# Performance work log

Measured on AMD Instinct MI355X. Metric: run time of the kernel, lower is better.

Reference implementation:

```python
import jax, jax.numpy as jnp
import numpy as np

B, T, C, HS, E, NR, P = 2, 2048, 1024, 64, 8, 6, 4
H = C // HS
FF = 4 * C
NT = E - NR


def _ln(x, w, b):
    m = x.mean(-1, keepdims=True)
    v = x.var(-1, keepdims=True)
    return (x - m) * jax.lax.rsqrt(v + 1e-5) * w + b


def _rwkv_scan(r, k, v, w):
    # r,k,v,w: (B,T,H,D); per-head linear-attention recurrence with channel decay
    def step(S, inp):
        r_t, k_t, v_t, w_t = inp  # (B,H,D)
        S = S * w_t[..., :, None] + k_t[..., :, None] * v_t[..., None, :]
        y = jnp.einsum('bhk,bhkv->bhv', r_t, S)
        return S, y
    Bb, Tt, Hh, Dd = r.shape
    S0 = jnp.zeros((Bb, Hh, Dd, Dd), r.dtype)
    xs = tuple(jnp.moveaxis(a, 1, 0) for a in (r, k, v, w))
    _, ys = jax.lax.scan(step, S0, xs)
    return jnp.moveaxis(ys, 0, 1)


def setup_inputs() -> dict:
    key = jax.random.key(0)
    ks = jax.random.split(key, 24)
    s = 1.0 / np.sqrt(C)
    n = lambda k, sh, sc: jax.random.normal(k, sh, jnp.float32) * sc
    return {
        'x': n(ks[0], (B, T, C), 1.0),
        'v_first': jnp.zeros((B, T, C), jnp.float32),
        'capital_shares': jax.random.uniform(ks[1], (E,), dtype=jnp.float32),
        'ln1_w': jnp.ones((C,), jnp.float32), 'ln1_b': jnp.zeros((C,), jnp.float32),
        'ln2_w': jnp.ones((C,), jnp.float32), 'ln2_b': jnp.zeros((C,), jnp.float32),
        'Wr': n(ks[2], (C, C), s), 'Wk': n(ks[3], (C, C), s),
        'Wv': n(ks[4], (C, C), s), 'Ww': n(ks[5], (C, C), s),
        'w_bias': 2.0 * jnp.ones((C,), jnp.float32),
        'Wo': n(ks[6], (C, C), s),
        'conf_w': n(ks[7], (E, C), s), 'conf_b': jnp.zeros((E,), jnp.float32),
        'Wd': n(ks[8], (C, 1), s), 'bd': jnp.zeros((1,), jnp.float32),
        'Wa': n(ks[9], (C, E), s), 'ba': jnp.zeros((E,), jnp.float32),
        'Wb': n(ks[10], (2 * C, P * C), 1.0 / np.sqrt(2 * C)),
        'ffn_Wr': n(ks[11], (NR, C, C), s),
        'ffn_Wk': n(ks[12], (NR, C, FF), s),
        'ffn_Wv': n(ks[13], (NR, FF, C), 1.0 / np.sqrt(FF)),
        'tr_Wq': n(ks[14], (NT, C, C), s), 'tr_Wk': n(ks[15], (NT, C, C), s),
        'tr_Wv': n(ks[16], (NT, C, C), s), 'tr_Wo': n(ks[17], (NT, C, C), s),
    }


def _forward(x, v_first, capital_shares, ln1_w, ln1_b, ln2_w, ln2_b,
             Wr, Wk, Wv, Ww, w_bias, Wo, conf_w, conf_b, Wd, bd, Wa, ba, Wb,
             ffn_Wr, ffn_Wk, ffn_Wv, tr_Wq, tr_Wk, tr_Wv, tr_Wo):
    # --- attention stage: ln1 -> RWKV7 TimeMix -> residual -> ln2 ---
    x_ln = _ln(x, ln1_w, ln1_b)
    r = (x_ln @ Wr).reshape(B, T, H, HS)
    k = (x_ln @ Wk).reshape(B, T, H, HS)
    v_flat = x_ln @ Wv
    v = v_flat.reshape(B, T, H, HS)
    w = jax.nn.sigmoid(x_ln @ Ww + w_bias).reshape(B, T, H, HS)  # decay in (0,1)
    rwkv_state = _rwkv_scan(r, k, v, w).reshape(B, T, C)
    att_out = rwkv_state @ Wo
    x_after_att = x + att_out
    h = _ln(x_after_att, ln2_w, ln2_b)
    # --- no-grad market routing: confidences + critic + top-2 auction ---
    rh = jax.lax.stop_gradient(h)
    conf = jax.nn.sigmoid(jnp.einsum('btc,ec->bte', rh, conf_w) + conf_b)  # (B,T,E)
    difficulty = jax.nn.softplus(rh @ Wd + bd)          # (B,T,1)
    affinity = rh @ Wa + ba                             # (B,T,E)
    subsidy = jax.nn.softmax(affinity, axis=-1)         # critic subsidy
    bids = conf * capital_shares + subsidy
    top_vals, winners = jax.lax.top_k(bids, 2)          # (B,T,2)
    weights = jax.lax.stop_gradient(jax.nn.softmax(top_vals, axis=-1))
    # --- bridge prefix for transformer experts ---
    BT = B * T
    flat_h = h.reshape(BT, C)
    flat_state = rwkv_state.reshape(BT, C)
    prefix = jnp.tanh(jnp.concatenate([flat_h, flat_state], -1) @ Wb).reshape(BT, P, C)
    # --- top-2 expert mixing: gate==0 for unselected tokens (same math as masked dispatch) ---
    final_out = jnp.zeros_like(h)
    scale = 1.0 / np.sqrt(HS)
    for e in range(E):
        gate = (weights * (winners == e)).sum(-1)  # (B,T)
        if e < NR:  # sparse RWKV FFN expert: relu^2 channel-mix with receptance gate
            kk = jax.nn.relu(h @ ffn_Wk[e]) ** 2
            out_e = jax.nn.sigmoid(h @ ffn_Wr[e]) * (kk @ ffn_Wv[e])
        else:       # linear transformer expert: cross-attend token over its bridge prefix
            t = e - NR
            q = (flat_h @ tr_Wq[t]).reshape(BT, H, HS)
            kp = (prefix @ tr_Wk[t]).reshape(BT, P, H, HS)
            vp = (prefix @ tr_Wv[t]).reshape(BT, P, H, HS)
            a = jax.nn.softmax(jnp.einsum('nhd,nphd->nhp', q, kp) * scale, -1)
            out_e = (jnp.einsum('nhp,nphd->nhd', a, vp).reshape(BT, C) @ tr_Wo[t]).reshape(B, T, C)
        final_out = final_out + gate[..., None] * out_e
    x_out = x_after_att + final_out
    return x_out, v_flat  # layer 0: v_first is set to the value projection


def reference(x, v_first, capital_shares, ln1_w, ln1_b, ln2_w, ln2_b,
              Wr, Wk, Wv, Ww, w_bias, Wo, conf_w, conf_b, Wd, bd, Wa, ba, Wb,
              ffn_Wr, ffn_Wk, ffn_Wv, tr_Wq, tr_Wk, tr_Wv, tr_Wo):
    return _forward(x, v_first, capital_shares, ln1_w, ln1_b, ln2_w, ln2_b,
                    Wr, Wk, Wv, Ww, w_bias, Wo, conf_w, conf_b, Wd, bd, Wa, ba, Wb,
                    ffn_Wr, ffn_Wk, ffn_Wv, tr_Wq, tr_Wk, tr_Wv, tr_Wo)
```

## Files before the change

kernel.cpp:

```cpp
#include <hip/hip_runtime.h>
#include <hip/hip_bf16.h>
#include <math.h>

#define Bn   2
#define Tn   2048
#define Cdim 1024
#define HSn  64
#define En   8
#define NRn  6
#define Pn   4
#define Hn   16
#define FFn  4096
#define NTn  2
#define BTn  4096
#define CHL  128
#define NCH  16

typedef __attribute__((ext_vector_type(8))) short bfrag;
typedef __attribute__((ext_vector_type(4))) float f32x4;

__device__ __forceinline__ void gl_lds16(const void* g, void* l) {
    __builtin_amdgcn_global_load_lds(
        (const __attribute__((address_space(1))) unsigned int*)g,
        (__attribute__((address_space(3))) unsigned int*)l, 16, 0, 0);
}

__device__ __forceinline__ float sigm(float v) { return 1.f / (1.f + expf(-v)); }

__global__ __launch_bounds__(256) void ln_kernel(const float* __restrict__ x,
                                                 const float* __restrict__ w,
                                                 const float* __restrict__ b,
                                                 float* __restrict__ out_f,
                                                 __hip_bfloat16* __restrict__ out_hi,
                                                 __hip_bfloat16* __restrict__ out_lo) {
    int row = blockIdx.x;
    const float* xr = x + (size_t)row * Cdim;
    int tid = threadIdx.x, l = tid & 63, wid = tid >> 6;
    float s = 0.f, s2 = 0.f;
    for (int c = tid; c < Cdim; c += 256) {
        float v = xr[c];
        s += v; s2 += v * v;
    }
#pragma unroll
    for (int off = 32; off > 0; off >>= 1) {
        s  += __shfl_xor(s, off);
        s2 += __shfl_xor(s2, off);
    }
    __shared__ float lnred[8];
    if (l == 0) { lnred[wid] = s; lnred[4 + wid] = s2; }
    __syncthreads();
    float ts  = lnred[0] + lnred[1] + lnred[2] + lnred[3];
    float ts2 = lnred[4] + lnred[5] + lnred[6] + lnred[7];
    float mean = ts / Cdim;
    float var  = ts2 / Cdim - mean * mean;
    float inv  = rsqrtf(var + 1e-5f);
    for (int c = tid; c < Cdim; c += 256) {
        float v = (xr[c] - mean) * inv * w[c] + b[c];
        size_t idx = (size_t)row * Cdim + c;
        if (out_f) out_f[idx] = v;
        if (out_hi) {
            __hip_bfloat16 hi = __float2bfloat16(v);
            out_hi[idx] = hi;
            if (out_lo) out_lo[idx] = __float2bfloat16(v - __bfloat162float(hi));
        }
    }
}

__global__ __launch_bounds__(256) void ln2_routing_kernel(
    const float* __restrict__ x, const float* __restrict__ w,
    const float* __restrict__ b, __hip_bfloat16* __restrict__ out_hi,
    const float* __restrict__ conf_w, const float* __restrict__ conf_b,
    const float* __restrict__ Wa, const float* __restrict__ ba,
    const float* __restrict__ cap, int* __restrict__ meta,
    int2* __restrict__ winfo, float2* __restrict__ gvals) {
    int row = blockIdx.x;
    const float* xr = x + (size_t)row * Cdim;
    int tid = threadIdx.x, l = tid & 63, wid = tid >> 6;
    float s = 0.f, s2 = 0.f;
    for (int c = tid; c < Cdim; c += 256) {
        float v = xr[c];
        s += v; s2 += v * v;
    }
#pragma unroll
    for (int off = 32; off > 0; off >>= 1) {
        s  += __shfl_xor(s, off);
        s2 += __shfl_xor(s2, off);
    }
    __shared__ float lnred[8];
    if (l == 0) { lnred[wid] = s; lnred[4 + wid] = s2; }
    __syncthreads();
    float ts  = lnred[0] + lnred[1] + lnred[2] + lnred[3];
    float ts2 = lnred[4] + lnred[5] + lnred[6] + lnred[7];
    float mean = ts / Cdim;
    float var  = ts2 / Cdim - mean * mean;
    float inv  = rsqrtf(var + 1e-5f);

    float pc[8], pa[8];
#pragma unroll
    for (int e = 0; e < 8; e++) { pc[e] = 0.f; pa[e] = 0.f; }
    for (int c = tid; c < Cdim; c += 256) {
        float hv = (xr[c] - mean) * inv * w[c] + b[c];
        out_hi[(size_t)row * Cdim + c] = __float2bfloat16(hv);
#pragma unroll
        for (int e = 0; e < 8; e++) {
            pc[e] += hv * conf_w[(size_t)e * Cdim + c];
            pa[e] += hv * Wa[(size_t)c * En + e];
        }
    }
#pragma unroll
    for (int off = 32; off > 0; off >>= 1) {
#pragma unroll
        for (int e = 0; e < 8; e++) {
            pc[e] += __shfl_xor(pc[e], off);
            pa[e] += __shfl_xor(pa[e], off);
        }
    }
    __shared__ float ered[4][16];
    if (l == 0) {
#pragma unroll
        for (int e = 0; e < 8; e++) {
            ered[wid][e]     = pc[e];
            ered[wid][8 + e] = pa[e];
        }
    }
    __syncthreads();
    if (tid == 0) {
        float conf[8], aff[8];
#pragma unroll
        for (int e = 0; e < 8; e++) {
            float vc = ered[0][e] + ered[1][e] + ered[2][e] + ered[3][e];
            float va = ered[0][8 + e] + ered[1][8 + e] + ered[2][8 + e] + ered[3][8 + e];
            conf[e] = sigm(vc + conf_b[e]);
            aff[e]  = va + ba[e];
        }
        float mx = aff[0];
#pragma unroll
        for (int e = 1; e < 8; e++) mx = fmaxf(mx, aff[e]);
        float se = 0.f, ex[8];
#pragma unroll
        for (int e = 0; e < 8; e++) { ex[e] = expf(aff[e] - mx); se += ex[e]; }
        float bids[8];
#pragma unroll
        for (int e = 0; e < 8; e++) bids[e] = conf[e] * cap[e] + ex[e] / se;
        int w0 = 0;
#pragma unroll
        for (int e = 1; e < 8; e++) if (bids[e] > bids[w0]) w0 = e;
        float b0 = bids[w0];
        int w1 = -1; float b1 = -1e30f;
#pragma unroll
        for (int e = 0; e < 8; e++) {
            if (e == w0) continue;
            if (w1 < 0 || bids[e] > b1) { w1 = e; b1 = bids[e]; }
        }
        float e1 = expf(b1 - b0);
        float g0 = 1.f / (1.f + e1);
        float g1 = e1 / (1.f + e1);
        winfo[row] = make_int2(w0, w1);
        gvals[row] = make_float2(g0, g1);
        atomicAdd(&meta[w0], 1);
        atomicAdd(&meta[w1], 1);
    }
}

__global__ __launch_bounds__(256) void convT_kernel(const float* __restrict__ W,
                                                    __hip_bfloat16* __restrict__ Wt,
                                                    int K, int N) {
    __shared__ float tile[32][33];
    int k0 = blockIdx.y * 32, n0 = blockIdx.x * 32;
    int tx = threadIdx.x, ty = threadIdx.y;
#pragma unroll
    for (int i = 0; i < 32; i += 8)
        tile[ty + i][tx] = W[(size_t)(k0 + ty + i) * N + n0 + tx];
    __syncthreads();
#pragma unroll
    for (int i = 0; i < 32; i += 8)
        Wt[(size_t)(n0 + ty + i) * K + k0 + tx] = __float2bfloat16(tile[tx][ty + i]);
}

__global__ __launch_bounds__(256) void convT_split_kernel(const float* __restrict__ W,
                                                          __hip_bfloat16* __restrict__ Wh,
                                                          __hip_bfloat16* __restrict__ Wl,
                                                          int K, int N) {
    __shared__ float tile[32][33];
    int k0 = blockIdx.y * 32, n0 = blockIdx.x * 32;
    int tx = threadIdx.x, ty = threadIdx.y;
#pragma unroll
    for (int i = 0; i < 32; i += 8)
        tile[ty + i][tx] = W[(size_t)(k0 + ty + i) * N + n0 + tx];
    __syncthreads();
#pragma unroll
    for (int i = 0; i < 32; i += 8) {
        float v = tile[tx][ty + i];
        __hip_bfloat16 hi = __float2bfloat16(v);
        size_t o = (size_t)(n0 + ty + i) * K + k0 + tx;
        Wh[o] = hi;
        Wl[o] = __float2bfloat16(v - __bfloat162float(hi));
    }
}

__global__ __launch_bounds__(256) void convT_split4_kernel(
    const float* __restrict__ W0, const float* __restrict__ W1,
    const float* __restrict__ W2, const float* __restrict__ W3,
    __hip_bfloat16* __restrict__ Wh, __hip_bfloat16* __restrict__ Wl) {
    int z = blockIdx.z;
    const float* W = (z == 0) ? W0 : (z == 1) ? W1 : (z == 2) ? W2 : W3;
    __hip_bfloat16* Whz = Wh + (size_t)z * Cdim * Cdim;
    __hip_bfloat16* Wlz = Wl + (size_t)z * Cdim * Cdim;
    __shared__ float tile[32][33];
    int k0 = blockIdx.y * 32, n0 = blockIdx.x * 32;
    int tx = threadIdx.x, ty = threadIdx.y;
#pragma unroll
    for (int i = 0; i < 32; i += 8)
        tile[ty + i][tx] = W[(size_t)(k0 + ty + i) * Cdim + n0 + tx];
    __syncthreads();
#pragma unroll
    for (int i = 0; i < 32; i += 8) {
        float v = tile[tx][ty + i];
        __hip_bfloat16 hi = __float2bfloat16(v);
        size_t o = (size_t)(n0 + ty + i) * Cdim + k0 + tx;
        Whz[o] = hi;
        Wlz[o] = __float2bfloat16(v - __bfloat162float(hi));
    }
}

__global__ __launch_bounds__(256) void convT_ffn_kernel(
    const float* __restrict__ Wr, const float* __restrict__ Wk,
    const float* __restrict__ Wv, __hip_bfloat16* __restrict__ dRK,
    __hip_bfloat16* __restrict__ dV) {
    int z = blockIdx.z;
    const float* src; __hip_bfloat16* dst; int srcLD, dstLD;
    if (z == 0) {
        src = Wr; dst = dRK; srcLD = 1024; dstLD = 1024;
    } else if (z < 5) {
        int s = z - 1;
        src = Wk + (size_t)s * 1024;
        dst = dRK + (size_t)(1024 + s * 1024) * 1024;
        srcLD = FFn; dstLD = 1024;
    } else {
        int s = z - 5;
        src = Wv + (size_t)s * 1024 * Cdim;
        dst = dV + (size_t)s * 1024;
        srcLD = Cdim; dstLD = FFn;
    }
    __shared__ float tile[32][33];
    int k0 = blockIdx.y * 32, n0 = blockIdx.x * 32;
    int tx = threadIdx.x, ty = threadIdx.y;
#pragma unroll
    for (int i = 0; i < 32; i += 8)
        tile[ty + i][tx] = src[(size_t)(k0 + ty + i) * srcLD + n0 + tx];
    __syncthreads();
#pragma unroll
    for (int i = 0; i < 32; i += 8)
        dst[(size_t)(n0 + ty + i) * dstLD + k0 + tx] = __float2bfloat16(tile[tx][ty + i]);
}

__global__ __launch_bounds__(256) void convT_tr8_kernel(
    const float* __restrict__ Wk, const float* __restrict__ Wv,
    const float* __restrict__ Wq, const float* __restrict__ Wo,
    __hip_bfloat16* __restrict__ dst) {
    int z = blockIdx.z;
    int t = z >> 2, j = z & 3;
    const float* srcs[4] = {Wk, Wv, Wq, Wo};
    const float* W = srcs[j] + (size_t)t * Cdim * Cdim;
    __hip_bfloat16* Wt = dst + (size_t)z * Cdim * Cdim;
    __shared__ float tile[32][33];
    int k0 = blockIdx.y * 32, n0 = blockIdx.x * 32;
    int tx = threadIdx.x, ty = threadIdx.y;
#pragma unroll
    for (int i = 0; i < 32; i += 8)
        tile[ty + i][tx] = W[(size_t)(k0 + ty + i) * Cdim + n0 + tx];
    __syncthreads();
#pragma unroll
    for (int i = 0; i < 32; i += 8)
        Wt[(size_t)(n0 + ty + i) * Cdim + k0 + tx] = __float2bfloat16(tile[tx][ty + i]);
}


enum { EP3_QKVW = 0, EP3_ADD = 1 };

template <int EP>
__global__ __launch_bounds__(256) void bgemm3_kernel(
    const __hip_bfloat16* __restrict__ Ah, const __hip_bfloat16* __restrict__ Al,
    const __hip_bfloat16* __restrict__ Bh, const __hip_bfloat16* __restrict__ Bl,
    float* __restrict__ o0, float* __restrict__ o1,
    float* __restrict__ o2, float* __restrict__ o3,
    int M, int N, int K, const float* __restrict__ aux) {
    __shared__ __align__(16) __hip_bfloat16 Ahs[8192], Als[8192], Bhs[8192], Bls[8192];
    int tid = threadIdx.x;
    int m0 = blockIdx.y * 128, n0 = blockIdx.x * 128;
    int l = tid & 63, wv = tid >> 6;
    int wm = (wv >> 1) * 64, wn = (wv & 1) * 64;
    int lr = l & 15, lq = l >> 4;

    f32x4 acc[4][4];
#pragma unroll
    for (int i = 0; i < 4; i++)
#pragma unroll
        for (int j = 0; j < 4; j++) acc[i][j] = (f32x4){0.f, 0.f, 0.f, 0.f};

    int srow = tid >> 3;
    int sq = (tid & 7) ^ (srow & 7);
    size_t arow = (size_t)(m0 + srow) * K + (sq << 3);
    size_t brow = (size_t)(n0 + srow) * K + (sq << 3);

    for (int kt = 0; kt < K; kt += 64) {
#pragma unroll
        for (int c = 0; c < 4; c++) {
            size_t go = (size_t)(c * 32) * K + kt;
            gl_lds16(Ah + arow + go, Ahs + c * 2048 + tid * 8);
            gl_lds16(Al + arow + go, Als + c * 2048 + tid * 8);
            gl_lds16(Bh + brow + go, Bhs + c * 2048 + tid * 8);
            gl_lds16(Bl + brow + go, Bls + c * 2048 + tid * 8);
        }
        __syncthreads();
#pragma unroll
        for (int kc = 0; kc < 64; kc += 32) {
            bfrag ah[4], al[4], bh[4], bl[4];
#pragma unroll
            for (int mi = 0; mi < 4; mi++) {
                int rr = wm + mi * 16 + lr;
                int off = rr * 64 + ((((kc >> 3) + lq) ^ (rr & 7)) << 3);
                ah[mi] = *(const bfrag*)&Ahs[off];
                al[mi] = *(const bfrag*)&Als[off];
            }
#pragma unroll
            for (int ni = 0; ni < 4; ni++) {
                int rr = wn + ni * 16 + lr;
                int off = rr * 64 + ((((kc >> 3) + lq) ^ (rr & 7)) << 3);
                bh[ni] = *(const bfrag*)&Bhs[off];
                bl[ni] = *(const bfrag*)&Bls[off];
            }
#pragma unroll
            for (int mi = 0; mi < 4; mi++)
#pragma unroll
                for (int ni = 0; ni < 4; ni++) {
                    acc[mi][ni] = __builtin_amdgcn_mfma_f32_16x16x32_bf16(ah[mi], bh[ni], acc[mi][ni], 0, 0, 0);
                    acc[mi][ni] = __builtin_amdgcn_mfma_f32_16x16x32_bf16(al[mi], bh[ni], acc[mi][ni], 0, 0, 0);
                    acc[mi][ni] = __builtin_amdgcn_mfma_f32_16x16x32_bf16(ah[mi], bl[ni], acc[mi][ni], 0, 0, 0);
                }
        }
        __syncthreads();
    }

#pragma unroll
    for (int mi = 0; mi < 4; mi++) {
#pragma unroll
        for (int r = 0; r < 4; r++) {
            int row = m0 + wm + mi * 16 + lq * 4 + r;
#pragma unroll
            for (int ni = 0; ni < 4; ni++) {
                int col = n0 + wn + ni * 16 + lr;
                float v = acc[mi][ni][r];
                if (EP == EP3_QKVW) {
                    int sel = col >> 10, cc = col & 1023;
                    size_t idx = (size_t)row * 1024 + cc;
                    if (sel == 0) o0[idx] = v;
                    else if (sel == 1) o1[idx] = v;
                    else if (sel == 2) o2[idx] = v;
                    else o3[idx] = sigm(v + aux[cc]);
                } else {
                    size_t idx = (size_t)row * N + col;
                    o0[idx] = aux[idx] + v;
                }
            }
        }
    }
}

enum { EP_TANHB = 0, EP_Q = 1, EP_MOE = 2, EP_MOEM = 3, EP_FFN1 = 4, EP_KV = 5 };

template <int EP>
__global__ __launch_bounds__(256) void bgemm_kernel(
    const __hip_bfloat16* __restrict__ A, const __hip_bfloat16* __restrict__ Bt,
    void* __restrict__ Cv, void* __restrict__ Cv2, int M, int N, int K,
    const int* __restrict__ meta, int e,
    const int* __restrict__ tokidx, const float* __restrict__ tokgate,
    const float* __restrict__ aux2) {
    const size_t CC_ = (size_t)Cdim * Cdim;
    int rows = M;
    int offA = 0;
    int outoff = 0;
    const __hip_bfloat16* Bp = Bt;
    const int* sidx = nullptr;
    const float* sgate = nullptr;
    if (meta) {
        if (EP == EP_TANHB) {
            rows = meta[6] + meta[7];
        } else if (EP == EP_KV) {
            int zx = blockIdx.z;
            rows = meta[6 + zx] * 4;
            offA = (meta[8 + 6 + zx] - meta[14]) * 4;
            outoff = offA;
            Bp = Bt + (size_t)(zx * 4) * CC_;
        } else if (EP == EP_Q) {
            int zx = blockIdx.z;
            rows = meta[6 + zx];
            offA = meta[8 + 6 + zx];
            outoff = meta[8 + 6 + zx] - meta[14];
            Bp = Bt + (size_t)(zx * 4 + 2) * CC_;
        } else if (EP == EP_MOE) {
            rows = meta[e];
            offA = meta[8 + e] - meta[14];
            sidx = tokidx + meta[8 + e];
            sgate = tokgate + meta[8 + e];
        } else if (EP == EP_MOEM) {
            rows = meta[e];
            sidx = tokidx + meta[8 + e];
            sgate = tokgate + meta[8 + e];
        } else {
            rows = meta[e];
            offA = meta[8 + e];
        }
    }
    int m0 = blockIdx.y * 128;
    if (m0 >= rows) return;

    __shared__ __align__(16) __hip_bfloat16 Asm[8192];
    __shared__ __align__(16) __hip_bfloat16 Bsm[8192];
    int tid = threadIdx.x;
    int n0 = blockIdx.x * 128;
    int l = tid & 63, wv = tid >> 6;
    int wm = (wv >> 1) * 64, wn = (wv & 1) * 64;
    int lr = l & 15, lq = l >> 4;

    f32x4 acc[4][4];
#pragma unroll
    for (int i = 0; i < 4; i++)
#pragma unroll
        for (int j = 0; j < 4; j++) acc[i][j] = (f32x4){0.f, 0.f, 0.f, 0.f};

    int srow = tid >> 3;
    int sq = (tid & 7) ^ (srow & 7);
    size_t arow = (size_t)(m0 + offA + srow) * K + (sq << 3);
    size_t brow = (size_t)(n0 + srow) * K + (sq << 3);

    int kbeg, kend;
    if (EP == EP_KV || EP == EP_Q) {
        kbeg = 0; kend = K;
    } else {
        int ks = K / gridDim.z;
        kbeg = blockIdx.z * ks; kend = kbeg + ks;
    }

    for (int kt = kbeg; kt < kend; kt += 64) {
#pragma unroll
        for (int c = 0; c < 4; c++) {
            size_t go = (size_t)(c * 32) * K + kt;
            gl_lds16(A + arow + go, Asm + c * 2048 + tid * 8);
            gl_lds16(Bp + brow + go, Bsm + c * 2048 + tid * 8);
        }
        __syncthreads();
#pragma unroll
        for (int kc = 0; kc < 64; kc += 32) {
            bfrag af[4], bf[4];
#pragma unroll
            for (int mi = 0; mi < 4; mi++) {
                int rr = wm + mi * 16 + lr;
                af[mi] = *(const bfrag*)&Asm[rr * 64 + ((((kc >> 3) + lq) ^ (rr & 7)) << 3)];
            }
#pragma unroll
            for (int ni = 0; ni < 4; ni++) {
                int rr = wn + ni * 16 + lr;
                bf[ni] = *(const bfrag*)&Bsm[rr * 64 + ((((kc >> 3) + lq) ^ (rr & 7)) << 3)];
            }
#pragma unroll
            for (int mi = 0; mi < 4; mi++)
#pragma unroll
                for (int ni = 0; ni < 4; ni++)
                    acc[mi][ni] = __builtin_amdgcn_mfma_f32_16x16x32_bf16(
                        af[mi], bf[ni], acc[mi][ni], 0, 0, 0);
        }
        __syncthreads();
    }

    float* Cf = (float*)Cv;
    __hip_bfloat16* Cb = (__hip_bfloat16*)Cv;
#pragma unroll
    for (int mi = 0; mi < 4; mi++) {
#pragma unroll
        for (int r = 0; r < 4; r++) {
            int row = m0 + wm + mi * 16 + lq * 4 + r;
            if (row >= rows) continue;
            int orow = row + outoff;
            int t = 0; float g = 0.f;
            if (EP == EP_MOE || EP == EP_MOEM) { t = sidx[row]; g = sgate[row]; }
#pragma unroll
            for (int ni = 0; ni < 4; ni++) {
                int col = n0 + wn + ni * 16 + lr;
                float v = acc[mi][ni][r];
                if (EP == EP_TANHB) {
                    Cb[(size_t)row * N + col] = __float2bfloat16(tanhf(v));
                } else if (EP == EP_Q) {
                    Cb[(size_t)orow * N + col] = __float2bfloat16(v);
                } else if (EP == EP_MOE) {
                    float* p = Cf + (size_t)t * 1024 + col;
                    *p = *p + g * v;
                } else if (EP == EP_MOEM) {
                    atomicAdd(Cf + (size_t)t * 1024 + col,
                              g * aux2[(size_t)row * 1024 + col] * v);
                } else if (EP == EP_FFN1) {
                    if ((col >> 10) == 0) {
                        Cf[(size_t)row * 1024 + col] = sigm(v);
                    } else {
                        float q = fmaxf(v, 0.f);
                        ((__hip_bfloat16*)Cv2)[(size_t)row * 4096 + col - 1024] =
                            __float2bfloat16(q * q);
                    }
                } else if (EP == EP_KV) {
                    if ((col >> 10) == 0)
                        Cb[(size_t)orow * 1024 + col] = __float2bfloat16(v);
                    else
                        ((__hip_bfloat16*)Cv2)[(size_t)orow * 1024 + col - 1024] =
                            __float2bfloat16(v);
                }
            }
        }
    }
}

__global__ __launch_bounds__(256) void scan_pass1(
    const float* __restrict__ k, const float* __restrict__ v,
    const float* __restrict__ w, float* __restrict__ Mbuf,
    float* __restrict__ Pbuf) {
    int c = blockIdx.x, bh = blockIdx.y;
    int b = bh >> 4, h = bh & 15;
    int tid = threadIdx.x, j = tid & 63, ig = tid >> 6;
    __shared__ float sbuf[2][3][64];
    float S[16], P[16];
#pragma unroll
    for (int ii = 0; ii < 16; ii++) { S[ii] = 0.f; P[ii] = 1.f; }

    size_t base = ((size_t)b * Tn + (size_t)c * CHL) * Cdim + (size_t)h * HSn + j;
    const float* srcs[3] = {k, v, w};
    const float* myp = (ig > 0) ? srcs[ig - 1] + base : k + base;

    const int CH = 8;
    float buf[CH];
#pragma unroll
    for (int u = 0; u < CH; u++) buf[u] = (ig > 0) ? myp[(size_t)u * Cdim] : 0.f;

    for (int tc = 0; tc < CHL; tc += CH) {
        float nbuf[CH];
#pragma unroll
        for (int u = 0; u < CH; u++) {
            int t2 = tc + CH + u;
            nbuf[u] = (ig > 0 && t2 < CHL) ? myp[(size_t)t2 * Cdim] : 0.f;
        }
#pragma unroll
        for (int u = 0; u < CH; u++) {
            int p = (tc + u) & 1;
            if (ig > 0) sbuf[p][ig - 1][j] = buf[u];
            __syncthreads();
            float vj = sbuf[p][1][j];
            const float* skp = sbuf[p][0];
            const float* swp = sbuf[p][2];
#pragma unroll
            for (int ii = 0; ii < 16; ii++) {
                int i = (ig << 4) + ii;
                float wi = swp[i];
                S[ii] = S[ii] * wi + skp[i] * vj;
                P[ii] *= wi;
            }
        }
#pragma unroll
        for (int u = 0; u < CH; u++) buf[u] = nbuf[u];
    }
    size_t mo = ((size_t)c * 32 + bh) * 4096;
#pragma unroll
    for (int ii = 0; ii < 16; ii++)
        Mbuf[mo + (size_t)((ig << 4) + ii) * 64 + j] = S[ii];
    if (j == 0) {
#pragma unroll
        for (int ii = 0; ii < 16; ii++)
            Pbuf[((size_t)c * 32 + bh) * 64 + (ig << 4) + ii] = P[ii];
    }
}

__global__ __launch_bounds__(256) void scan_pass2(
    const float* __restrict__ Mbuf, const float* __restrict__ Pbuf,
    float* __restrict__ Sinb) {
    int bh = blockIdx.y;
    int idx = blockIdx.x * 256 + threadIdx.x;
    int i = idx >> 6;
    float S = 0.f;
    for (int c = 0; c < NCH; c++) {
        size_t o = ((size_t)c * 32 + bh);
        Sinb[o * 4096 + idx] = S;
        S = Pbuf[o * 64 + i] * S + Mbuf[o * 4096 + idx];
    }
}

__global__ __launch_bounds__(256) void scan_pass3(
    const float* __restrict__ r, const float* __restrict__ k,
    const float* __restrict__ v, const float* __restrict__ w,
    const float* __restrict__ Sinb,
    __hip_bfloat16* __restrict__ sh, __hip_bfloat16* __restrict__ sl) {
    int c = blockIdx.x, bh = blockIdx.y;
    int b = bh >> 4, h = bh & 15;
    int tid = threadIdx.x, j = tid & 63, ig = tid >> 6;
    __shared__ float sbuf[2][4][64];
    __shared__ float red[2][4][64];
    float S[16];
    size_t so = ((size_t)c * 32 + bh) * 4096;
#pragma unroll
    for (int ii = 0; ii < 16; ii++)
        S[ii] = Sinb[so + (size_t)((ig << 4) + ii) * 64 + j];

    size_t base = ((size_t)b * Tn + (size_t)c * CHL) * Cdim + (size_t)h * HSn + j;
    const float* srcs[4] = {r, k, v, w};
    const float* myp = srcs[ig] + base;

    const int CH = 8;
    float buf[CH];
#pragma unroll
    for (int u = 0; u < CH; u++) buf[u] = myp[(size_t)u * Cdim];
    float part_prev = 0.f;

    for (int tc = 0; tc < CHL; tc += CH) {
        float nbuf[CH];
#pragma unroll
        for (int u = 0; u < CH; u++) {
            int t2 = tc + CH + u;
            nbuf[u] = (t2 < CHL) ? myp[(size_t)t2 * Cdim] : 0.f;
        }
#pragma unroll
        for (int u = 0; u < CH; u++) {
            int t = tc + u;
            int p = t & 1;
            sbuf[p][ig][j] = buf[u];
            red[p][ig][j] = part_prev;
            __syncthreads();
            if (ig == 0 && t > 0) {
                float val = red[p][0][j] + red[p][1][j] + red[p][2][j] + red[p][3][j];
                __hip_bfloat16 hi = __float2bfloat16(val);
                size_t pos = base + (size_t)(t - 1) * Cdim;
                sh[pos] = hi;
                sl[pos] = __float2bfloat16(val - __bfloat162float(hi));
            }
            float vj = sbuf[p][2][j];
            const float* srp = sbuf[p][0];
            const float* skp = sbuf[p][1];
            const float* swp = sbuf[p][3];
            float part = 0.f;
#pragma unroll
            for (int ii = 0; ii < 16; ii++) {
                int i = (ig << 4) + ii;
                S[ii] = S[ii] * swp[i] + skp[i] * vj;
                part += srp[i] * S[ii];
            }
            part_prev = part;
        }
#pragma unroll
        for (int u = 0; u < CH; u++) buf[u] = nbuf[u];
    }
    red[0][ig][j] = part_prev;
    __syncthreads();
    if (ig == 0) {
        float val = red[0][0][j] + red[0][1][j] + red[0][2][j] + red[0][3][j];
        __hip_bfloat16 hi = __float2bfloat16(val);
        size_t pos = base + (size_t)(CHL - 1) * Cdim;
        sh[pos] = hi;
        sl[pos] = __float2bfloat16(val - __bfloat162float(hi));
    }
}

__global__ __launch_bounds__(256) void assign_kernel(
    const int2* __restrict__ winfo, const float2* __restrict__ gvals,
    int* __restrict__ meta, int* __restrict__ tokidx,
    float* __restrict__ tokgate, int2* __restrict__ posbuf) {
    int e = blockIdx.x;
    int tid = threadIdx.x;
    __shared__ int scn[256];
    int base = 0;
    for (int e2 = 0; e2 < e; ++e2) base += meta[e2];
    if (tid == 0) meta[8 + e] = base;
    for (int c = 0; c < BTn; c += 256) {
        int t = c + tid;
        int2 w = winfo[t];
        int m0 = (w.x == e) ? 1 : 0;
        int m1 = (w.y == e) ? 1 : 0;
        int cnt = m0 + m1;
        scn[tid] = cnt;
        __syncthreads();
        for (int st = 1; st < 256; st <<= 1) {
            int vv = (tid >= st) ? scn[tid - st] : 0;
            __syncthreads();
            scn[tid] += vv;
            __syncthreads();
        }
        int excl = scn[tid] - cnt;
        int tot = scn[255];
        if (m0) {
            int p = base + excl;
            tokidx[p] = t; tokgate[p] = gvals[t].x; posbuf[t].x = p;
        }
        if (m1) {
            int p = base + excl;
            tokidx[p] = t; tokgate[p] = gvals[t].y; posbuf[t].y = p;
        }
        base += tot;
        __syncthreads();
    }
}

__global__ __launch_bounds__(256) void gather_kernel(
    const __hip_bfloat16* __restrict__ h_bf, const __hip_bfloat16* __restrict__ st,
    const int2* __restrict__ winfo, const int2* __restrict__ posbuf,
    const int* __restrict__ meta,
    __hip_bfloat16* __restrict__ hc, __hip_bfloat16* __restrict__ hsc) {
    int t = blockIdx.x;
    int tid = threadIdx.x;
    int2 w = winfo[t];
    int2 p = posbuf[t];
    int off6 = meta[14];
    ushort4 hv = ((const ushort4*)(h_bf + (size_t)t * 1024))[tid];
    ((ushort4*)(hc + (size_t)p.x * 1024))[tid] = hv;
    ((ushort4*)(hc + (size_t)p.y * 1024))[tid] = hv;
    if (w.x >= 6) {
        int lp = p.x - off6;
        ((ushort4*)(hsc + (size_t)lp * 2048))[tid] = hv;
        ((ushort4*)(hsc + (size_t)lp * 2048 + 1024))[tid] =
            ((const ushort4*)(st + (size_t)t * 1024))[tid];
    }
    if (w.y >= 6) {
        int lp = p.y - off6;
        ((ushort4*)(hsc + (size_t)lp * 2048))[tid] = hv;
        ((ushort4*)(hsc + (size_t)lp * 2048 + 1024))[tid] =
            ((const ushort4*)(st + (size_t)t * 1024))[tid];
    }
}

__global__ __launch_bounds__(256) void tr_attn_kernel(
    const __hip_bfloat16* __restrict__ qc, const __hip_bfloat16* __restrict__ kpc,
    const __hip_bfloat16* __restrict__ vpc, __hip_bfloat16* __restrict__ attnc,
    const int* __restrict__ meta) {
    int cnt = meta[6] + meta[7];
    int idx = blockIdx.x * 4 + (threadIdx.x >> 6);
    int lane = threadIdx.x & 63;
    int n = idx >> 4, h = idx & 15;
    if (n >= cnt) return;
    float qd = __bfloat162float(qc[(size_t)n * Cdim + (size_t)h * HSn + lane]);
    float s[4];
#pragma unroll
    for (int p = 0; p < 4; p++) {
        float t = qd * __bfloat162float(kpc[((size_t)n * Pn + p) * Cdim + (size_t)h * HSn + lane]);
        for (int off = 32; off > 0; off >>= 1) t += __shfl_down(t, off);
        s[p] = __shfl(t, 0);
    }
    const float scale = 0.125f;
    float mx = fmaxf(fmaxf(s[0], s[1]), fmaxf(s[2], s[3])) * scale;
    float es = 0.f, a[4];
#pragma unroll
    for (int p = 0; p < 4; p++) { a[p] = expf(s[p] * scale - mx); es += a[p]; }
    float o = 0.f;
#pragma unroll
    for (int p = 0; p < 4; p++)
        o += (a[p] / es) * __bfloat162float(vpc[((size_t)n * Pn + p) * Cdim + (size_t)h * HSn + lane]);
    attnc[(size_t)n * Cdim + (size_t)h * HSn + lane] = __float2bfloat16(o);
}

extern "C" void kernel_launch(void* const* d_in, const int* in_sizes, int n_in,
                              void* d_out, int out_size, void* d_ws, size_t ws_size,
                              hipStream_t stream) {
    const float* x      = (const float*)d_in[0];
    const float* cap    = (const float*)d_in[2];
    const float* ln1_w  = (const float*)d_in[3];
    const float* ln1_b  = (const float*)d_in[4];
    const float* ln2_w  = (const float*)d_in[5];
    const float* ln2_b  = (const float*)d_in[6];
    const float* Wr     = (const float*)d_in[7];
    const float* Wk     = (const float*)d_in[8];
    const float* Wv     = (const float*)d_in[9];
    const float* Ww     = (const float*)d_in[10];
    const float* w_bias = (const float*)d_in[11];
    const float* Wo     = (const float*)d_in[12];
    const float* conf_w = (const float*)d_in[13];
    const float* conf_b = (const float*)d_in[14];
    const float* Wa     = (const float*)d_in[17];
    const float* ba     = (const float*)d_in[18];
    const float* Wb     = (const float*)d_in[19];
    const float* ffn_Wr = (const float*)d_in[20];
    const float* ffn_Wk = (const float*)d_in[21];
    const float* ffn_Wv = (const float*)d_in[22];
    const float* tr_Wq  = (const float*)d_in[23];
    const float* tr_Wk  = (const float*)d_in[24];
    const float* tr_Wv  = (const float*)d_in[25];
    const float* tr_Wo  = (const float*)d_in[26];

    float* xout  = (float*)d_out;
    float* vflat = (float*)d_out + (size_t)BTn * Cdim;

    char* ws = (char*)d_ws;
    const size_t MB = 1ull << 20;
    __hip_bfloat16* xln_hi  = (__hip_bfloat16*)(ws + 0 * MB);
    __hip_bfloat16* xln_lo  = (__hip_bfloat16*)(ws + 8 * MB);
    __hip_bfloat16* Wall_hi = (__hip_bfloat16*)(ws + 16 * MB);
    __hip_bfloat16* Wall_lo = (__hip_bfloat16*)(ws + 24 * MB);
    float*          rbuf    = (float*)(ws + 32 * MB);
    float*          kbuf    = (float*)(ws + 48 * MB);
    float*          wbuf    = (float*)(ws + 64 * MB);
    float*          Pbuf    = (float*)(ws + 80 * MB);
    __hip_bfloat16* Wo_hi   = (__hip_bfloat16*)(ws + 81 * MB);
    __hip_bfloat16* Wo_lo   = (__hip_bfloat16*)(ws + 83 * MB);
    float*          Mbuf    = (float*)(ws + 0 * MB);
    float*          Sinb    = (float*)(ws + 8 * MB);
    __hip_bfloat16* st_hi   = (__hip_bfloat16*)(ws + 16 * MB);
    __hip_bfloat16* st_lo   = (__hip_bfloat16*)(ws + 24 * MB);
    __hip_bfloat16* h_bf    = (__hip_bfloat16*)(ws + 48 * MB);
    __hip_bfloat16* hc      = (__hip_bfloat16*)(ws + 56 * MB);
    __hip_bfloat16* hsc     = (__hip_bfloat16*)(ws + 74 * MB);
    __hip_bfloat16* Wt_b    = (__hip_bfloat16*)(ws + 108 * MB);
    __hip_bfloat16* prefixc = (__hip_bfloat16*)(ws + 124 * MB);
    __hip_bfloat16* eWall   = (__hip_bfloat16*)(ws + 0 * MB);
    __hip_bfloat16* eWv_t   = (__hip_bfloat16*)(ws + 10 * MB);
    float*          rg      = (float*)(ws + 18 * MB);
    __hip_bfloat16* kk      = (__hip_bfloat16*)(ws + 74 * MB);
    __hip_bfloat16* vpc     = (__hip_bfloat16*)(ws + 0 * MB);
    __hip_bfloat16* tkv     = (__hip_bfloat16*)(ws + 34 * MB);
    __hip_bfloat16* kpc     = (__hip_bfloat16*)(ws + 74 * MB);
    __hip_bfloat16* qc      = (__hip_bfloat16*)(ws + 108 * MB);
    __hip_bfloat16* attnc   = (__hip_bfloat16*)(ws + 192 * MB);
    int*    meta    = (int*)(ws + 200 * MB);
    int*    tokidx  = (int*)(ws + 200 * MB + (64 << 10));
    float*  tokgate = (float*)(ws + 200 * MB + (128 << 10));
    int2*   winfo   = (int2*)(ws + 200 * MB + (192 << 10));
    float2* gvals   = (float2*)(ws + 200 * MB + (256 << 10));
    int2*   posbuf  = (int2*)(ws + 200 * MB + (320 << 10));
    (void)ws_size; (void)in_sizes; (void)n_in; (void)out_size;

    dim3 blk(256);
    dim3 tblk(32, 8);
    auto grid  = [](int M, int N) { return dim3(N / 128, M / 128); };
    auto tgrid = [](int K, int N) { return dim3(N / 32, K / 32); };
    const size_t CC = (size_t)Cdim * Cdim;

    hipMemsetAsync(meta, 0, 96, stream);
    convT_split4_kernel<<<dim3(32, 32, 4), tblk, 0, stream>>>(Wr, Wk, Wv, Ww, Wall_hi, Wall_lo);
    convT_split_kernel<<<tgrid(Cdim, Cdim), tblk, 0, stream>>>(Wo, Wo_hi, Wo_lo, Cdim, Cdim);
    convT_kernel<<<tgrid(2 * Cdim, Pn * Cdim), tblk, 0, stream>>>(Wb, Wt_b, 2 * Cdim, Pn * Cdim);

    ln_kernel<<<BTn, blk, 0, stream>>>(x, ln1_w, ln1_b, nullptr, xln_hi, xln_lo);
    bgemm3_kernel<EP3_QKVW><<<grid(BTn, 4 * Cdim), blk, 0, stream>>>(
        xln_hi, xln_lo, Wall_hi, Wall_lo, rbuf, kbuf, vflat, wbuf, BTn, 4 * Cdim, Cdim, w_bias);
    scan_pass1<<<dim3(NCH, 32), blk, 0, stream>>>(kbuf, vflat, wbuf, Mbuf, Pbuf);
    scan_pass2<<<dim3(16, 32), blk, 0, stream>>>(Mbuf, Pbuf, Sinb);
    scan_pass3<<<dim3(NCH, 32), blk, 0, stream>>>(rbuf, kbuf, vflat, wbuf, Sinb, st_hi, st_lo);
    bgemm3_kernel<EP3_ADD><<<grid(BTn, Cdim), blk, 0, stream>>>(
        st_hi, st_lo, Wo_hi, Wo_lo, xout, nullptr, nullptr, nullptr, BTn, Cdim, Cdim, x);
    ln2_routing_kernel<<<BTn, blk, 0, stream>>>(
        xout, ln2_w, ln2_b, h_bf, conf_w, conf_b, Wa, ba, cap, meta, winfo, gvals);
    assign_kernel<<<dim3(8), blk, 0, stream>>>(winfo, gvals, meta, tokidx, tokgate, posbuf);
    gather_kernel<<<BTn, blk, 0, stream>>>(h_bf, st_hi, winfo, posbuf, meta, hc, hsc);
    bgemm_kernel<EP_TANHB><<<grid(2 * BTn, Pn * Cdim), blk, 0, stream>>>(
        hsc, Wt_b, prefixc, nullptr, 2 * BTn, Pn * Cdim, 2 * Cdim, meta, 0, nullptr, nullptr, nullptr);
    for (int e = 0; e < NRn; e++) {
        convT_ffn_kernel<<<dim3(32, 32, 9), tblk, 0, stream>>>(
            ffn_Wr + (size_t)e * CC, ffn_Wk + (size_t)e * Cdim * FFn,
            ffn_Wv + (size_t)e * FFn * Cdim, eWall, eWv_t);
        bgemm_kernel<EP_FFN1><<<grid(BTn, 5 * Cdim), blk, 0, stream>>>(
            hc, eWall, rg, kk, BTn, 5 * Cdim, Cdim, meta, e, nullptr, nullptr, nullptr);
        bgemm_kernel<EP_MOEM><<<dim3(Cdim / 128, BTn / 128, 2), blk, 0, stream>>>(
            kk, eWv_t, xout, nullptr, BTn, Cdim, FFn, meta, e, tokidx, tokgate, rg);
    }
    convT_tr8_kernel<<<dim3(32, 32, 8), tblk, 0, stream>>>(tr_Wk, tr_Wv, tr_Wq, tr_Wo, tkv);
    bgemm_kernel<EP_KV><<<dim3(16, 128, 2), blk, 0, stream>>>(
        prefixc, tkv, kpc, vpc, 4 * BTn, 2 * Cdim, Cdim, meta, 6, nullptr, nullptr, nullptr);
    bgemm_kernel<EP_Q><<<dim3(8, 32, 2), blk, 0, stream>>>(
        hc, tkv, qc, nullptr, BTn, Cdim, Cdim, meta, 6, nullptr, nullptr, nullptr);
    tr_attn_kernel<<<(BTn * Hn) / 4, blk, 0, stream>>>(qc, kpc, vpc, attnc, meta);
    for (int t = 0; t < NTn; t++) {
        bgemm_kernel<EP_MOE><<<grid(BTn, Cdim), blk, 0, stream>>>(
            attnc, tkv + (size_t)(4 * t + 3) * CC, xout, nullptr,
            BTn, Cdim, Cdim, meta, 6 + t, tokidx, tokgate, nullptr);
    }
}
```

Baseline: 1.621 ms.

## Vectorize layernorm and transposes, merge weight conversions and batch transformer output GEMMs

Layernorm and routing kernels now load and store four floats per thread instead of striding scalar loops, and the weight transpose kernels use 64x64 tiles with float4 loads and ushort4 bf16 stores. The Wr/Wk/Wv/Ww/Wo split conversions are merged into one launch. The two transformer-expert output GEMMs become a single launch indexed by grid z, which switches their write to atomicAdd because both experts can update the same token. The assign kernel replaces its barrier-heavy shared-memory scan with a wave shuffle scan. Together these aim to cut memory transactions and launch count, at the cost of atomic contention and possible nondeterministic summation order.

```diff
diff --git a/kernel.cpp b/kernel.cpp
--- a/kernel.cpp
+++ b/kernel.cpp
@@ -36,11 +36,10 @@
     int row = blockIdx.x;
     const float* xr = x + (size_t)row * Cdim;
     int tid = threadIdx.x, l = tid & 63, wid = tid >> 6;
-    float s = 0.f, s2 = 0.f;
-    for (int c = tid; c < Cdim; c += 256) {
-        float v = xr[c];
-        s += v; s2 += v * v;
-    }
+    int c4 = tid << 2;
+    float4 v = *(const float4*)&xr[c4];
+    float s  = v.x + v.y + v.z + v.w;
+    float s2 = v.x * v.x + v.y * v.y + v.z * v.z + v.w * v.w;
 #pragma unroll
     for (int off = 32; off > 0; off >>= 1) {
         s  += __shfl_xor(s, off);
@@ -54,14 +53,28 @@
     float mean = ts / Cdim;
     float var  = ts2 / Cdim - mean * mean;
     float inv  = rsqrtf(var + 1e-5f);
-    for (int c = tid; c < Cdim; c += 256) {
-        float v = (xr[c] - mean) * inv * w[c] + b[c];
-        size_t idx = (size_t)row * Cdim + c;
-        if (out_f) out_f[idx] = v;
-        if (out_hi) {
-            __hip_bfloat16 hi = __float2bfloat16(v);
-            out_hi[idx] = hi;
-            if (out_lo) out_lo[idx] = __float2bfloat16(v - __bfloat162float(hi));
+    float4 wv4 = *(const float4*)&w[c4];
+    float4 bv4 = *(const float4*)&b[c4];
+    float h0 = (v.x - mean) * inv * wv4.x + bv4.x;
+    float h1 = (v.y - mean) * inv * wv4.y + bv4.y;
+    float h2 = (v.z - mean) * inv * wv4.z + bv4.z;
+    float h3 = (v.w - mean) * inv * wv4.w + bv4.w;
+    size_t idx = (size_t)row * Cdim + c4;
+    if (out_f) {
+        float4 of = {h0, h1, h2, h3};
+        *(float4*)&out_f[idx] = of;
+    }
+    if (out_hi) {
+        __hip_bfloat16 hh[4] = {__float2bfloat16(h0), __float2bfloat16(h1),
+                                __float2bfloat16(h2), __float2bfloat16(h3)};
+        *(ushort4*)&out_hi[idx] = *(ushort4*)hh;
+        if (out_lo) {
+            __hip_bfloat16 ll[4] = {
+                __float2bfloat16(h0 - __bfloat162float(hh[0])),
+                __float2bfloat16(h1 - __bfloat162float(hh[1])),
+                __float2bfloat16(h2 - __bfloat162float(hh[2])),
+                __float2bfloat16(h3 - __bfloat162float(hh[3]))};
+            *(ushort4*)&out_lo[idx] = *(ushort4*)ll;
         }
     }
 }
@@ -76,11 +89,10 @@
     int row = blockIdx.x;
     const float* xr = x + (size_t)row * Cdim;
     int tid = threadIdx.x, l = tid & 63, wid = tid >> 6;
-    float s = 0.f, s2 = 0.f;
-    for (int c = tid; c < Cdim; c += 256) {
-        float v = xr[c];
-        s += v; s2 += v * v;
-    }
+    int c4 = tid << 2;
+    float4 v = *(const float4*)&xr[c4];
+    float s  = v.x + v.y + v.z + v.w;
+    float s2 = v.x * v.x + v.y * v.y + v.z * v.z + v.w * v.w;
 #pragma unroll
     for (int off = 32; off > 0; off >>= 1) {
         s  += __shfl_xor(s, off);
@@ -94,18 +106,34 @@
     float mean = ts / Cdim;
     float var  = ts2 / Cdim - mean * mean;
     float inv  = rsqrtf(var + 1e-5f);
-
+    float4 wv4 = *(const float4*)&w[c4];
+    float4 bv4 = *(const float4*)&b[c4];
+    float h0 = (v.x - mean) * inv * wv4.x + bv4.x;
+    float h1 = (v.y - mean) * inv * wv4.y + bv4.y;
+    float h2 = (v.z - mean) * inv * wv4.z + bv4.z;
+    float h3 = (v.w - mean) * inv * wv4.w + bv4.w;
+    {
+        __hip_bfloat16 hh[4] = {__float2bfloat16(h0), __float2bfloat16(h1),
+                                __float2bfloat16(h2), __float2bfloat16(h3)};
+        *(ushort4*)&out_hi[(size_t)row * Cdim + c4] = *(ushort4*)hh;
+    }
     float pc[8], pa[8];
 #pragma unroll
     for (int e = 0; e < 8; e++) { pc[e] = 0.f; pa[e] = 0.f; }
-    for (int c = tid; c < Cdim; c += 256) {
-        float hv = (xr[c] - mean) * inv * w[c] + b[c];
-        out_hi[(size_t)row * Cdim + c] = __float2bfloat16(hv);
-#pragma unroll
-        for (int e = 0; e < 8; e++) {
-            pc[e] += hv * conf_w[(size_t)e * Cdim + c];
-            pa[e] += hv * Wa[(size_t)c * En + e];
-        }
+#pragma unroll
+    for (int e = 0; e < 8; e++) {
+        float4 cw = *(const float4*)&conf_w[(size_t)e * Cdim + c4];
+        pc[e] = h0 * cw.x + h1 * cw.y + h2 * cw.z + h3 * cw.w;
+    }
+    float hv4[4] = {h0, h1, h2, h3};
+#pragma unroll
+    for (int j = 0; j < 4; j++) {
+        float4 wa0 = *(const float4*)&Wa[(size_t)(c4 + j) * En];
+        float4 wa1 = *(const float4*)&Wa[(size_t)(c4 + j) * En + 4];
+        pa[0] += hv4[j] * wa0.x; pa[1] += hv4[j] * wa0.y;
+        pa[2] += hv4[j] * wa0.z; pa[3] += hv4[j] * wa0.w;
+        pa[4] += hv4[j] * wa1.x; pa[5] += hv4[j] * wa1.y;
+        pa[6] += hv4[j] * wa1.z; pa[7] += hv4[j] * wa1.w;
     }
 #pragma unroll
     for (int off = 32; off > 0; off >>= 1) {
@@ -162,71 +190,80 @@
     }
 }
 
-__global__ __launch_bounds__(256) void convT_kernel(const float* __restrict__ W,
-                                                    __hip_bfloat16* __restrict__ Wt,
-                                                    int K, int N) {
-    __shared__ float tile[32][33];
-    int k0 = blockIdx.y * 32, n0 = blockIdx.x * 32;
-    int tx = threadIdx.x, ty = threadIdx.y;
-#pragma unroll
-    for (int i = 0; i < 32; i += 8)
-        tile[ty + i][tx] = W[(size_t)(k0 + ty + i) * N + n0 + tx];
+template <bool SPLIT>
+__device__ __forceinline__ void convT64_core(
+    const float* __restrict__ src, int srcLD,
+    __hip_bfloat16* __restrict__ dh, __hip_bfloat16* __restrict__ dl, int dstLD,
+    int k0, int n0, float* tile) {
+    int tid = threadIdx.x;
+#pragma unroll
+    for (int i = 0; i < 4; i++) {
+        int f = i * 256 + tid;
+        int row = f >> 4;
+        int c4 = (f & 15) << 2;
+        float4 v = *(const float4*)&src[(size_t)(k0 + row) * srcLD + n0 + c4];
+        tile[row * 65 + c4 + 0] = v.x;
+        tile[row * 65 + c4 + 1] = v.y;
+        tile[row * 65 + c4 + 2] = v.z;
+        tile[row * 65 + c4 + 3] = v.w;
+    }
     __syncthreads();
 #pragma unroll
-    for (int i = 0; i < 32; i += 8)
-        Wt[(size_t)(n0 + ty + i) * K + k0 + tx] = __float2bfloat16(tile[tx][ty + i]);
-}
-
-__global__ __launch_bounds__(256) void convT_split_kernel(const float* __restrict__ W,
-                                                          __hip_bfloat16* __restrict__ Wh,
-                                                          __hip_bfloat16* __restrict__ Wl,
-                                                          int K, int N) {
-    __shared__ float tile[32][33];
-    int k0 = blockIdx.y * 32, n0 = blockIdx.x * 32;
-    int tx = threadIdx.x, ty = threadIdx.y;
-#pragma unroll
-    for (int i = 0; i < 32; i += 8)
-        tile[ty + i][tx] = W[(size_t)(k0 + ty + i) * N + n0 + tx];
-    __syncthreads();
-#pragma unroll
-    for (int i = 0; i < 32; i += 8) {
-        float v = tile[tx][ty + i];
-        __hip_bfloat16 hi = __float2bfloat16(v);
-        size_t o = (size_t)(n0 + ty + i) * K + k0 + tx;
-        Wh[o] = hi;
-        Wl[o] = __float2bfloat16(v - __bfloat162float(hi));
-    }
-}
-
-__global__ __launch_bounds__(256) void convT_split4_kernel(
+    for (int i = 0; i < 4; i++) {
+        int g = i * 256 + tid;
+        int orow = g >> 4;
+        int oc4 = (g & 15) << 2;
+        float a = tile[(oc4 + 0) * 65 + orow];
+        float b = tile[(oc4 + 1) * 65 + orow];
+        float c = tile[(oc4 + 2) * 65 + orow];
+        float d = tile[(oc4 + 3) * 65 + orow];
+        __hip_bfloat16 hh[4] = {__float2bfloat16(a), __float2bfloat16(b),
+                                __float2bfloat16(c), __float2bfloat16(d)};
+        size_t o = (size_t)(n0 + orow) * dstLD + k0 + oc4;
+        *(ushort4*)&dh[o] = *(ushort4*)hh;
+        if (SPLIT) {
+            __hip_bfloat16 ll[4] = {
+                __float2bfloat16(a - __bfloat162float(hh[0])),
+                __float2bfloat16(b - __bfloat162float(hh[1])),
+                __float2bfloat16(c - __bfloat162float(hh[2])),
+                __float2bfloat16(d - __bfloat162float(hh[3]))};
+            *(ushort4*)&dl[o] = *(ushort4*)ll;
+        }
+    }
+}
+
+__global__ __launch_bounds__(256) void convT_split5_kernel(
     const float* __restrict__ W0, const float* __restrict__ W1,
     const float* __restrict__ W2, const float* __restrict__ W3,
-    __hip_bfloat16* __restrict__ Wh, __hip_bfloat16* __restrict__ Wl) {
+    const float* __restrict__ W4,
+    __hip_bfloat16* __restrict__ Wall_h, __hip_bfloat16* __restrict__ Wall_l,
+    __hip_bfloat16* __restrict__ Wo_h, __hip_bfloat16* __restrict__ Wo_l) {
+    __shared__ float tile[64 * 65];
     int z = blockIdx.z;
-    const float* W = (z == 0) ? W0 : (z == 1) ? W1 : (z == 2) ? W2 : W3;
-    __hip_bfloat16* Whz = Wh + (size_t)z * Cdim * Cdim;
-    __hip_bfloat16* Wlz = Wl + (size_t)z * Cdim * Cdim;
-    __shared__ float tile[32][33];
-    int k0 = blockIdx.y * 32, n0 = blockIdx.x * 32;
-    int tx = threadIdx.x, ty = threadIdx.y;
-#pragma unroll
-    for (int i = 0; i < 32; i += 8)
-        tile[ty + i][tx] = W[(size_t)(k0 + ty + i) * Cdim + n0 + tx];
-    __syncthreads();
-#pragma unroll
-    for (int i = 0; i < 32; i += 8) {
-        float v = tile[tx][ty + i];
-        __hip_bfloat16 hi = __float2bfloat16(v);
-        size_t o = (size_t)(n0 + ty + i) * Cdim + k0 + tx;
-        Whz[o] = hi;
-        Wlz[o] = __float2bfloat16(v - __bfloat162float(hi));
-    }
+    const float* srcs[5] = {W0, W1, W2, W3, W4};
+    const float* src = srcs[z];
+    __hip_bfloat16 *dh, *dl;
+    if (z < 4) {
+        dh = Wall_h + (size_t)z * Cdim * Cdim;
+        dl = Wall_l + (size_t)z * Cdim * Cdim;
+    } else {
+        dh = Wo_h; dl = Wo_l;
+    }
+    convT64_core<true>(src, Cdim, dh, dl, Cdim, blockIdx.y * 64, blockIdx.x * 64, tile);
+}
+
+__global__ __launch_bounds__(256) void convT64_kernel(const float* __restrict__ W,
+                                                      __hip_bfloat16* __restrict__ Wt,
+                                                      int K, int N) {
+    __shared__ float tile[64 * 65];
+    convT64_core<false>(W, N, Wt, nullptr, K, blockIdx.y * 64, blockIdx.x * 64, tile);
 }
 
 __global__ __launch_bounds__(256) void convT_ffn_kernel(
     const float* __restrict__ Wr, const float* __restrict__ Wk,
     const float* __restrict__ Wv, __hip_bfloat16* __restrict__ dRK,
     __hip_bfloat16* __restrict__ dV) {
+    __shared__ float tile[64 * 65];
     int z = blockIdx.z;
     const float* src; __hip_bfloat16* dst; int srcLD, dstLD;
     if (z == 0) {
@@ -242,37 +279,22 @@
         dst = dV + (size_t)s * 1024;
         srcLD = Cdim; dstLD = FFn;
     }
-    __shared__ float tile[32][33];
-    int k0 = blockIdx.y * 32, n0 = blockIdx.x * 32;
-    int tx = threadIdx.x, ty = threadIdx.y;
-#pragma unroll
-    for (int i = 0; i < 32; i += 8)
-        tile[ty + i][tx] = src[(size_t)(k0 + ty + i) * srcLD + n0 + tx];
-    __syncthreads();
-#pragma unroll
-    for (int i = 0; i < 32; i += 8)
-        dst[(size_t)(n0 + ty + i) * dstLD + k0 + tx] = __float2bfloat16(tile[tx][ty + i]);
+    convT64_core<false>(src, srcLD, dst, nullptr, dstLD,
+                        blockIdx.y * 64, blockIdx.x * 64, tile);
 }
 
 __global__ __launch_bounds__(256) void convT_tr8_kernel(
     const float* __restrict__ Wk, const float* __restrict__ Wv,
     const float* __restrict__ Wq, const float* __restrict__ Wo,
     __hip_bfloat16* __restrict__ dst) {
+    __shared__ float tile[64 * 65];
     int z = blockIdx.z;
     int t = z >> 2, j = z & 3;
     const float* srcs[4] = {Wk, Wv, Wq, Wo};
     const float* W = srcs[j] + (size_t)t * Cdim * Cdim;
     __hip_bfloat16* Wt = dst + (size_t)z * Cdim * Cdim;
-    __shared__ float tile[32][33];
-    int k0 = blockIdx.y * 32, n0 = blockIdx.x * 32;
-    int tx = threadIdx.x, ty = threadIdx.y;
-#pragma unroll
-    for (int i = 0; i < 32; i += 8)
-        tile[ty + i][tx] = W[(size_t)(k0 + ty + i) * Cdim + n0 + tx];
-    __syncthreads();
-#pragma unroll
-    for (int i = 0; i < 32; i += 8)
-        Wt[(size_t)(n0 + ty + i) * Cdim + k0 + tx] = __float2bfloat16(tile[tx][ty + i]);
+    convT64_core<false>(W, Cdim, Wt, nullptr, Cdim,
+                        blockIdx.y * 64, blockIdx.x * 64, tile);
 }
 
 
@@ -399,10 +421,12 @@
             outoff = meta[8 + 6 + zx] - meta[14];
             Bp = Bt + (size_t)(zx * 4 + 2) * CC_;
         } else if (EP == EP_MOE) {
-            rows = meta[e];
-            offA = meta[8 + e] - meta[14];
-            sidx = tokidx + meta[8 + e];
-            sgate = tokgate + meta[8 + e];
+            int zx = blockIdx.z;
+            rows = meta[6 + zx];
+            offA = meta[8 + 6 + zx] - meta[14];
+            sidx = tokidx + meta[8 + 6 + zx];
+            sgate = tokgate + meta[8 + 6 + zx];
+            Bp = Bt + (size_t)(zx * 4 + 3) * CC_;
         } else if (EP == EP_MOEM) {
             rows = meta[e];
             sidx = tokidx + meta[8 + e];
@@ -435,7 +459,7 @@
     size_t brow = (size_t)(n0 + srow) * K + (sq << 3);
 
     int kbeg, kend;
-    if (EP == EP_KV || EP == EP_Q) {
+    if (EP == EP_KV || EP == EP_Q || EP == EP_MOE) {
         kbeg = 0; kend = K;
     } else {
         int ks = K / gridDim.z;
@@ -493,8 +517,7 @@
                 } else if (EP == EP_Q) {
                     Cb[(size_t)orow * N + col] = __float2bfloat16(v);
                 } else if (EP == EP_MOE) {
-                    float* p = Cf + (size_t)t * 1024 + col;
-                    *p = *p + g * v;
+                    atomicAdd(Cf + (size_t)t * 1024 + col, g * v);
                 } else if (EP == EP_MOEM) {
                     atomicAdd(Cf + (size_t)t * 1024 + col,
                               g * aux2[(size_t)row * 1024 + col] * v);
@@ -669,8 +692,8 @@
     int* __restrict__ meta, int* __restrict__ tokidx,
     float* __restrict__ tokgate, int2* __restrict__ posbuf) {
     int e = blockIdx.x;
-    int tid = threadIdx.x;
-    __shared__ int scn[256];
+    int tid = threadIdx.x, l = tid & 63, wid = tid >> 6;
+    __shared__ int wsum[4];
     int base = 0;
     for (int e2 = 0; e2 < e; ++e2) base += meta[e2];
     if (tid == 0) meta[8 + e] = base;
@@ -680,24 +703,21 @@
         int m0 = (w.x == e) ? 1 : 0;
         int m1 = (w.y == e) ? 1 : 0;
         int cnt = m0 + m1;
-        scn[tid] = cnt;
+        int xs = cnt;
+#pragma unroll
+        for (int off = 1; off < 64; off <<= 1) {
+            int vv = __shfl_up(xs, off);
+            if (l >= off) xs += vv;
+        }
+        if (l == 63) wsum[wid] = xs;
         __syncthreads();
-        for (int st = 1; st < 256; st <<= 1) {
-            int vv = (tid >= st) ? scn[tid - st] : 0;
-            __syncthreads();
-            scn[tid] += vv;
-            __syncthreads();
-        }
-        int excl = scn[tid] - cnt;
-        int tot = scn[255];
-        if (m0) {
-            int p = base + excl;
-            tokidx[p] = t; tokgate[p] = gvals[t].x; posbuf[t].x = p;
-        }
-        if (m1) {
-            int p = base + excl;
-            tokidx[p] = t; tokgate[p] = gvals[t].y; posbuf[t].y = p;
-        }
+        int pre = 0;
+#pragma unroll
+        for (int wj = 0; wj < 4; wj++) if (wj < wid) pre += wsum[wj];
+        int tot = wsum[0] + wsum[1] + wsum[2] + wsum[3];
+        int p = base + pre + xs - cnt;
+        if (m0) { tokidx[p] = t; tokgate[p] = gvals[t].x; posbuf[t].x = p; }
+        if (m1) { tokidx[p] = t; tokgate[p] = gvals[t].y; posbuf[t].y = p; }
         base += tot;
         __syncthreads();
     }
@@ -829,15 +849,13 @@
     (void)ws_size; (void)in_sizes; (void)n_in; (void)out_size;
 
     dim3 blk(256);
-    dim3 tblk(32, 8);
-    auto grid  = [](int M, int N) { return dim3(N / 128, M / 128); };
-    auto tgrid = [](int K, int N) { return dim3(N / 32, K / 32); };
+    auto grid = [](int M, int N) { return dim3(N / 128, M / 128); };
     const size_t CC = (size_t)Cdim * Cdim;
 
     hipMemsetAsync(meta, 0, 96, stream);
-    convT_split4_kernel<<<dim3(32, 32, 4), tblk, 0, stream>>>(Wr, Wk, Wv, Ww, Wall_hi, Wall_lo);
-    convT_split_kernel<<<tgrid(Cdim, Cdim), tblk, 0, stream>>>(Wo, Wo_hi, Wo_lo, Cdim, Cdim);
-    convT_kernel<<<tgrid(2 * Cdim, Pn * Cdim), tblk, 0, stream>>>(Wb, Wt_b, 2 * Cdim, Pn * Cdim);
+    convT_split5_kernel<<<dim3(16, 16, 5), blk, 0, stream>>>(
+        Wr, Wk, Wv, Ww, Wo, Wall_hi, Wall_lo, Wo_hi, Wo_lo);
+    convT64_kernel<<<dim3(64, 32), blk, 0, stream>>>(Wb, Wt_b, 2 * Cdim, Pn * Cdim);
 
     ln_kernel<<<BTn, blk, 0, stream>>>(x, ln1_w, ln1_b, nullptr, xln_hi, xln_lo);
     bgemm3_kernel<EP3_QKVW><<<grid(BTn, 4 * Cdim), blk, 0, stream>>>(
@@ -854,7 +872,7 @@
     bgemm_kernel<EP_TANHB><<<grid(2 * BTn, Pn * Cdim), blk, 0, stream>>>(
         hsc, Wt_b, prefixc, nullptr, 2 * BTn, Pn * Cdim, 2 * Cdim, meta, 0, nullptr, nullptr, nullptr);
     for (int e = 0; e < NRn; e++) {
-        convT_ffn_kernel<<<dim3(32, 32, 9), tblk, 0, stream>>>(
+        convT_ffn_kernel<<<dim3(16, 16, 9), blk, 0, stream>>>(
             ffn_Wr + (size_t)e * CC, ffn_Wk + (size_t)e * Cdim * FFn,
             ffn_Wv + (size_t)e * FFn * Cdim, eWall, eWv_t);
         bgemm_kernel<EP_FFN1><<<grid(BTn, 5 * Cdim), blk, 0, stream>>>(
@@ -862,15 +880,12 @@
         bgemm_kernel<EP_MOEM><<<dim3(Cdim / 128, BTn / 128, 2), blk, 0, stream>>>(
             kk, eWv_t, xout, nullptr, BTn, Cdim, FFn, meta, e, tokidx, tokgate, rg);
     }
-    convT_tr8_kernel<<<dim3(32, 32, 8), tblk, 0, stream>>>(tr_Wk, tr_Wv, tr_Wq, tr_Wo, tkv);
+    convT_tr8_kernel<<<dim3(16, 16, 8), blk, 0, stream>>>(tr_Wk, tr_Wv, tr_Wq, tr_Wo, tkv);
     bgemm_kernel<EP_KV><<<dim3(16, 128, 2), blk, 0, stream>>>(
         prefixc, tkv, kpc, vpc, 4 * BTn, 2 * Cdim, Cdim, meta, 6, nullptr, nullptr, nullptr);
     bgemm_kernel<EP_Q><<<dim3(8, 32, 2), blk, 0, stream>>>(
         hc, tkv, qc, nullptr, BTn, Cdim, Cdim, meta, 6, nullptr, nullptr, nullptr);
     tr_attn_kernel<<<(BTn * Hn) / 4, blk, 0, stream>>>(qc, kpc, vpc, attnc, meta);
-    for (int t = 0; t < NTn; t++) {
-        bgemm_kernel<EP_MOE><<<grid(BTn, Cdim), blk, 0, stream>>>(
-            attnc, tkv + (size_t)(4 * t + 3) * CC, xout, nullptr,
-            BTn, Cdim, Cdim, meta, 6 + t, tokidx, tokgate, nullptr);
-    }
-}
+    bgemm_kernel<EP_MOE><<<dim3(8, 32, 2), blk, 0, stream>>>(
+        attnc, tkv, xout, nullptr, BTn, Cdim, Cdim, meta, 6, tokidx, tokgate, nullptr);
+}
```

After: 1.593 ms. Within noise of the previous version (-1.7%).
